# Kernel tuning notes

Measured on AMD Instinct MI355X. Metric: run time of the kernel, lower is better.

The kernel has to match this reference:

```python
import jax, jax.numpy as jnp
import numpy as np

N_EMBD = 768
N_HEAD = 12
HEAD_DIM = N_EMBD // N_HEAD
B, T = 2, 2048
EPS = 1e-5


def setup_inputs() -> dict:
    key = jax.random.key(0)
    ks = jax.random.split(key, 16)
    s = 0.02
    return {
        "x": jax.random.normal(ks[0], (B, T, N_EMBD), dtype=jnp.float32),
        "ln1_g": jnp.ones((N_EMBD,), jnp.float32),
        "ln1_b": jnp.zeros((N_EMBD,), jnp.float32),
        "W_attn": jax.random.normal(ks[1], (N_EMBD, 3 * N_EMBD), jnp.float32) * s,
        "b_attn": jnp.zeros((3 * N_EMBD,), jnp.float32),
        "W_cproj": jax.random.normal(ks[2], (N_EMBD, N_EMBD), jnp.float32) * s,
        "b_cproj": jnp.zeros((N_EMBD,), jnp.float32),
        "ln2_g": jnp.ones((N_EMBD,), jnp.float32),
        "ln2_b": jnp.zeros((N_EMBD,), jnp.float32),
        "W_fc": jax.random.normal(ks[3], (N_EMBD, 4 * N_EMBD), jnp.float32) * s,
        "b_fc": jnp.zeros((4 * N_EMBD,), jnp.float32),
        "W_mproj": jax.random.normal(ks[4], (4 * N_EMBD, N_EMBD), jnp.float32) * s,
        "b_mproj": jnp.zeros((N_EMBD,), jnp.float32),
    }


def _layernorm(x, g, b):
    mu = jnp.mean(x, axis=-1, keepdims=True)
    var = jnp.mean(jnp.square(x - mu), axis=-1, keepdims=True)
    return (x - mu) * jax.lax.rsqrt(var + EPS) * g + b


def _attention(h, W_attn, b_attn, W_cproj, b_cproj):
    Bx, Tx, C = h.shape
    qkv = h @ W_attn + b_attn  # [B, T, 3C]
    q, k, v = jnp.split(qkv, 3, axis=-1)
    # [B, H, T, D]
    def split_heads(t):
        return t.reshape(Bx, Tx, N_HEAD, HEAD_DIM).transpose(0, 2, 1, 3)
    q, k, v = split_heads(q), split_heads(k), split_heads(v)
    att = jnp.einsum("bhqd,bhkd->bhqk", q, k) / np.sqrt(HEAD_DIM).astype(np.float32)
    causal = jnp.tril(jnp.ones((Tx, Tx), dtype=bool))
    att = jnp.where(causal, att, jnp.float32(-jnp.inf))
    att = jax.nn.softmax(att, axis=-1)
    y = jnp.einsum("bhqk,bhkd->bhqd", att, v)
    y = y.transpose(0, 2, 1, 3).reshape(Bx, Tx, C)
    return y @ W_cproj + b_cproj


def _mlp(h, W_fc, b_fc, W_mproj, b_mproj):
    return jax.nn.gelu(h @ W_fc + b_fc, approximate=False) @ W_mproj + b_mproj


def reference(x, ln1_g, ln1_b, W_attn, b_attn, W_cproj, b_cproj,
              ln2_g, ln2_b, W_fc, b_fc, W_mproj, b_mproj):
    x = x + _attention(_layernorm(x, ln1_g, ln1_b), W_attn, b_attn, W_cproj, b_cproj)
    x = x + _mlp(_layernorm(x, ln2_g, ln2_b), W_fc, b_fc, W_mproj, b_mproj)
    return x
```

## Files before the change

### kernel.cpp

```cpp
#include <hip/hip_runtime.h>
#include <cstdint>
#include <cstddef>

#define B_ 2
#define T_ 2048
#define C_ 768
#define H_ 12
#define D_ 64

typedef __attribute__((ext_vector_type(8))) short s16x8;
typedef __attribute__((ext_vector_type(4))) float fx4;

static __device__ __forceinline__ unsigned short f2bf(float f) {
  unsigned u = __builtin_bit_cast(unsigned, f);
  unsigned r = u + 0x7fffu + ((u >> 16) & 1u);
  return (unsigned short)(r >> 16);
}
static __device__ __forceinline__ unsigned short f2bf_trunc(float f) {
  return (unsigned short)(__builtin_bit_cast(unsigned, f) >> 16);
}

static __device__ __forceinline__ void glds16(const unsigned short* g, unsigned short* l) {
  __builtin_amdgcn_global_load_lds(
      (const __attribute__((address_space(1))) void*)(g),
      (__attribute__((address_space(3))) void*)(l), 16, 0, 0);
}

__global__ __launch_bounds__(256) void transpose_cast(
    const float* __restrict__ W, unsigned short* __restrict__ Wt, int R, int C) {
  __shared__ float tile[32][33];
  int tx = threadIdx.x & 31;
  int ty = threadIdx.x >> 5;
  int c0 = blockIdx.x * 32, r0 = blockIdx.y * 32;
#pragma unroll
  for (int i = 0; i < 4; ++i)
    tile[ty + i * 8][tx] = W[(size_t)(r0 + ty + i * 8) * C + (c0 + tx)];
  __syncthreads();
#pragma unroll
  for (int i = 0; i < 4; ++i)
    Wt[(size_t)(c0 + ty + i * 8) * R + (r0 + tx)] = f2bf(tile[tx][ty + i * 8]);
}

__global__ __launch_bounds__(256) void layernorm_bf16(
    const float* __restrict__ X, const float* __restrict__ g,
    const float* __restrict__ bb, unsigned short* __restrict__ O) {
  int row = blockIdx.x, tid = threadIdx.x;
  const float* xr = X + (size_t)row * C_;
  float v0 = xr[tid], v1 = xr[tid + 256], v2 = xr[tid + 512];
  float s = v0 + v1 + v2;
  float s2 = v0 * v0 + v1 * v1 + v2 * v2;
#pragma unroll
  for (int off = 1; off < 64; off <<= 1) {
    s += __shfl_xor(s, off);
    s2 += __shfl_xor(s2, off);
  }
  __shared__ float ps[8];
  int wv = tid >> 6;
  if ((tid & 63) == 0) { ps[wv] = s; ps[wv + 4] = s2; }
  __syncthreads();
  s = ps[0] + ps[1] + ps[2] + ps[3];
  s2 = ps[4] + ps[5] + ps[6] + ps[7];
  float mu = s * (1.f / C_);
  float var = s2 * (1.f / C_) - mu * mu;
  float rstd = rsqrtf(var + 1e-5f);
  unsigned short* orow = O + (size_t)row * C_;
  orow[tid]       = f2bf((v0 - mu) * rstd * g[tid]       + bb[tid]);
  orow[tid + 256] = f2bf((v1 - mu) * rstd * g[tid + 256] + bb[tid + 256]);
  orow[tid + 512] = f2bf((v2 - mu) * rstd * g[tid + 512] + bb[tid + 512]);
}

template <int BM, int BN, int BK, int MODE>
__global__ __launch_bounds__(256) void gemm_db(
    const unsigned short* __restrict__ A, const unsigned short* __restrict__ Bt,
    const float* __restrict__ bias, const float* __restrict__ resid,
    float* __restrict__ outF, unsigned short* __restrict__ outB,
    unsigned short* __restrict__ qO, unsigned short* __restrict__ kO,
    unsigned short* __restrict__ vtO, int M, int N, int K) {
  constexpr int AT = BM / 32;
  constexpr int BT = BN / 32;
  constexpr int KS = BK / 32;
  constexpr int CA = BM * BK / 2048;
  constexpr int CB = BN * BK / 2048;
  constexpr int ASZ = BM * BK, BSZ = BN * BK;
  constexpr bool SWIZ = (BK == 64);
  __shared__ __align__(16) unsigned short As[2 * ASZ];
  __shared__ __align__(16) unsigned short Bs[2 * BSZ];
  int tid = threadIdx.x;
  int wv = tid >> 6, lane = tid & 63, quad = lane >> 4, l15 = lane & 15;
  int wm = wv >> 1, wn = wv & 1;
  int m0, n0;
  if (MODE == 1) { m0 = blockIdx.x * BM; n0 = blockIdx.y * BN; }
  else           { n0 = blockIdx.x * BN; m0 = blockIdx.y * BM; }
  fx4 acc[AT][BT];
#pragma unroll
  for (int i = 0; i < AT; ++i)
#pragma unroll
    for (int j = 0; j < BT; ++j) acc[i][j] = fx4{0.f, 0.f, 0.f, 0.f};

  int nk = K / BK;
#pragma unroll
  for (int i = 0; i < CA; ++i) {
    int e = (i * 256 + tid) * 8;
    int row = e / BK, col = e & (BK - 1);
    if (SWIZ) col = (((col >> 3) ^ (row & 7)) << 3);
    glds16(&A[(size_t)(m0 + row) * K + col], &As[(i * 256 + (tid & ~63)) * 8]);
  }
#pragma unroll
  for (int i = 0; i < CB; ++i) {
    int e = (i * 256 + tid) * 8;
    int row = e / BK, col = e & (BK - 1);
    if (SWIZ) col = (((col >> 3) ^ (row & 7)) << 3);
    glds16(&Bt[(size_t)(n0 + row) * K + col], &Bs[(i * 256 + (tid & ~63)) * 8]);
  }
  for (int kt = 0; kt < nk; ++kt) {
    int cur = kt & 1;
    __syncthreads();
    if (kt + 1 < nk) {
      int kb = (kt + 1) * BK;
      int nxt = cur ^ 1;
#pragma unroll
      for (int i = 0; i < CA; ++i) {
        int e = (i * 256 + tid) * 8;
        int row = e / BK, col = e & (BK - 1);
        if (SWIZ) col = (((col >> 3) ^ (row & 7)) << 3);
        glds16(&A[(size_t)(m0 + row) * K + kb + col],
               &As[nxt * ASZ + (i * 256 + (tid & ~63)) * 8]);
      }
#pragma unroll
      for (int i = 0; i < CB; ++i) {
        int e = (i * 256 + tid) * 8;
        int row = e / BK, col = e & (BK - 1);
        if (SWIZ) col = (((col >> 3) ^ (row & 7)) << 3);
        glds16(&Bt[(size_t)(n0 + row) * K + kb + col],
               &Bs[nxt * BSZ + (i * 256 + (tid & ~63)) * 8]);
      }
    }
#pragma unroll
    for (int ks = 0; ks < KS; ++ks) {
      s16x8 af[AT], bf[BT];
#pragma unroll
      for (int mt = 0; mt < AT; ++mt) {
        int r = wm * (BM / 2) + mt * 16 + l15;
        int c = ks * 32 + quad * 8;
        if (SWIZ) c = (((c >> 3) ^ (r & 7)) << 3);
        af[mt] = *(const s16x8*)&As[cur * ASZ + r * BK + c];
      }
#pragma unroll
      for (int nt = 0; nt < BT; ++nt) {
        int r = wn * (BN / 2) + nt * 16 + l15;
        int c = ks * 32 + quad * 8;
        if (SWIZ) c = (((c >> 3) ^ (r & 7)) << 3);
        bf[nt] = *(const s16x8*)&Bs[cur * BSZ + r * BK + c];
      }
#pragma unroll
      for (int mt = 0; mt < AT; ++mt)
#pragma unroll
        for (int nt = 0; nt < BT; ++nt)
          acc[mt][nt] = __builtin_amdgcn_mfma_f32_16x16x32_bf16(af[mt], bf[nt], acc[mt][nt], 0, 0, 0);
    }
  }

#pragma unroll
  for (int mt = 0; mt < AT; ++mt)
#pragma unroll
    for (int nt = 0; nt < BT; ++nt) {
      int mb = m0 + wm * (BM / 2) + mt * 16 + quad * 4;
      int n = n0 + wn * (BN / 2) + nt * 16 + l15;
      if (MODE == 0) {
        int which = n / C_;
        int within = n - which * C_;
        int hd = within >> 6, d = within & 63;
        int bbx = mb >> 11, t = mb & 2047;
        size_t bh = (size_t)(bbx * H_ + hd);
        float b = bias[n];
        if (which == 2) {
          unsigned v01 = (unsigned)f2bf(acc[mt][nt][0] + b) |
                         ((unsigned)f2bf(acc[mt][nt][1] + b) << 16);
          unsigned v23 = (unsigned)f2bf(acc[mt][nt][2] + b) |
                         ((unsigned)f2bf(acc[mt][nt][3] + b) << 16);
          *(uint2*)&vtO[(bh * D_ + d) * T_ + t] = uint2{v01, v23};
        } else {
          unsigned short* dst = (which == 0) ? qO : kO;
#pragma unroll
          for (int r = 0; r < 4; ++r)
            dst[(bh * T_ + t + r) * D_ + d] = f2bf(acc[mt][nt][r] + b);
        }
      } else if (MODE == 1) {
#pragma unroll
        for (int r = 0; r < 4; ++r) {
          int m = mb + r;
          float v = acc[mt][nt][r] + bias[n];
          outF[(size_t)m * N + n] = resid[(size_t)m * N + n] + v;
        }
      } else {
#pragma unroll
        for (int r = 0; r < 4; ++r) {
          int m = mb + r;
          float v = acc[mt][nt][r] + bias[n];
          float gl = 0.5f * v * (1.f + erff(v * 0.70710678118654752f));
          outB[(size_t)m * N + n] = f2bf(gl);
        }
      }
    }
}

__global__ __launch_bounds__(256) void attn_fused(
    const unsigned short* __restrict__ Q, const unsigned short* __restrict__ Kg,
    const unsigned short* __restrict__ Vt, unsigned short* __restrict__ Y) {
  __shared__ __align__(16) unsigned short Ks[64 * 72];
  __shared__ __align__(16) unsigned short Vs[64 * 72];
  __shared__ __align__(16) unsigned short Ps[4][16 * 72];
  int tid = threadIdx.x;
  int wv = tid >> 6, lane = tid & 63, quad = lane >> 4, l15 = lane & 15;
  int l = blockIdx.x;
  int w = l >> 8, c = l & 255;
  int i = c & 31;
  int bh = w * 8 + (c >> 5);
  int qt;
  if (w == 0)      qt = i;
  else if (w == 1) qt = (i + 16) & 31;
  else             qt = (i < 16) ? (30 - 2 * i) : (63 - 2 * i);
  int bbx = bh / H_, hh = bh - bbx * H_;
  int q0 = qt * 64;
  size_t base = (size_t)bh * T_ * D_;
  size_t vbase = (size_t)bh * D_ * T_;
  int qrow = q0 + wv * 16 + l15;
  s16x8 qf0 = *(const s16x8*)&Q[base + (size_t)qrow * D_ + quad * 8];
  s16x8 qf1 = *(const s16x8*)&Q[base + (size_t)qrow * D_ + 32 + quad * 8];
  float lsum[4];
  fx4 oacc[4];
#pragma unroll
  for (int t = 0; t < 4; ++t) {
    lsum[t] = 0.f;
    oacc[t] = fx4{0.f, 0.f, 0.f, 0.f};
  }
  int r0s = tid >> 3;
  int c8 = (tid & 7) * 8;
  uint4 ka, kc, va, vc;
  {
    ka = *(const uint4*)&Kg[base + (size_t)r0s * D_ + c8];
    kc = *(const uint4*)&Kg[base + (size_t)(r0s + 32) * D_ + c8];
    va = *(const uint4*)&Vt[vbase + (size_t)r0s * T_ + c8];
    vc = *(const uint4*)&Vt[vbase + (size_t)(r0s + 32) * T_ + c8];
  }
  for (int kb = 0; kb <= qt; ++kb) {
    int k0 = kb * 64;
    __syncthreads();
    *(uint4*)&Ks[r0s * 72 + c8] = ka;
    *(uint4*)&Ks[(r0s + 32) * 72 + c8] = kc;
    *(uint4*)&Vs[r0s * 72 + c8] = va;
    *(uint4*)&Vs[(r0s + 32) * 72 + c8] = vc;
    __syncthreads();
    if (kb < qt) {
      int kn = k0 + 64;
      ka = *(const uint4*)&Kg[base + (size_t)(kn + r0s) * D_ + c8];
      kc = *(const uint4*)&Kg[base + (size_t)(kn + r0s + 32) * D_ + c8];
      va = *(const uint4*)&Vt[vbase + (size_t)r0s * T_ + kn + c8];
      vc = *(const uint4*)&Vt[vbase + (size_t)(r0s + 32) * T_ + kn + c8];
    }
    fx4 sc[4];
#pragma unroll
    for (int nt = 0; nt < 4; ++nt) {
      sc[nt] = fx4{0.f, 0.f, 0.f, 0.f};
      s16x8 kf0 = *(const s16x8*)&Ks[(nt * 16 + l15) * 72 + quad * 8];
      s16x8 kf1 = *(const s16x8*)&Ks[(nt * 16 + l15) * 72 + 32 + quad * 8];
      sc[nt] = __builtin_amdgcn_mfma_f32_16x16x32_bf16(qf0, kf0, sc[nt], 0, 0, 0);
      sc[nt] = __builtin_amdgcn_mfma_f32_16x16x32_bf16(qf1, kf1, sc[nt], 0, 0, 0);
    }
    bool diag = (kb == qt);
    unsigned short* pw = &Ps[wv][0];
#pragma unroll
    for (int nt = 0; nt < 4; ++nt)
#pragma unroll
      for (int r = 0; r < 4; ++r) {
        float p;
        if (diag && (k0 + nt * 16 + l15) > (q0 + wv * 16 + quad * 4 + r)) {
          p = 0.f;
        } else {
          p = __expf(sc[nt][r] * 0.125f);
        }
        lsum[r] += p;
        pw[(quad * 4 + r) * 72 + nt * 16 + l15] = f2bf_trunc(p);
      }
    s16x8 pa0 = *(const s16x8*)&pw[l15 * 72 + quad * 8];
    s16x8 pa1 = *(const s16x8*)&pw[l15 * 72 + 32 + quad * 8];
#pragma unroll
    for (int nt = 0; nt < 4; ++nt) {
      s16x8 vf0 = *(const s16x8*)&Vs[(nt * 16 + l15) * 72 + quad * 8];
      s16x8 vf1 = *(const s16x8*)&Vs[(nt * 16 + l15) * 72 + 32 + quad * 8];
      oacc[nt] = __builtin_amdgcn_mfma_f32_16x16x32_bf16(pa0, vf0, oacc[nt], 0, 0, 0);
      oacc[nt] = __builtin_amdgcn_mfma_f32_16x16x32_bf16(pa1, vf1, oacc[nt], 0, 0, 0);
    }
  }
#pragma unroll
  for (int r = 0; r < 4; ++r) {
#pragma unroll
    for (int off = 1; off < 16; off <<= 1) lsum[r] += __shfl_xor(lsum[r], off);
  }
#pragma unroll
  for (int nt = 0; nt < 4; ++nt)
#pragma unroll
    for (int r = 0; r < 4; ++r) {
      float o = oacc[nt][r] / lsum[r];
      int token = bbx * T_ + q0 + wv * 16 + quad * 4 + r;
      Y[(size_t)token * C_ + hh * D_ + nt * 16 + l15] = f2bf(o);
    }
}

extern "C" void kernel_launch(void* const* d_in, const int* in_sizes, int n_in,
                              void* d_out, int out_size, void* d_ws, size_t ws_size,
                              hipStream_t stream) {
  const float* x      = (const float*)d_in[0];
  const float* ln1g   = (const float*)d_in[1];
  const float* ln1b   = (const float*)d_in[2];
  const float* Wattn  = (const float*)d_in[3];
  const float* battn  = (const float*)d_in[4];
  const float* Wcproj = (const float*)d_in[5];
  const float* bcproj = (const float*)d_in[6];
  const float* ln2g   = (const float*)d_in[7];
  const float* ln2b   = (const float*)d_in[8];
  const float* Wfc    = (const float*)d_in[9];
  const float* bfc    = (const float*)d_in[10];
  const float* Wmproj = (const float*)d_in[11];
  const float* bmproj = (const float*)d_in[12];
  float* out = (float*)d_out;
  char* ws = (char*)d_ws;

  unsigned short* WattnT  = (unsigned short*)(ws + 0);
  unsigned short* WcprojT = (unsigned short*)(ws + 3538944);
  unsigned short* WfcT    = (unsigned short*)(ws + 4718592);
  unsigned short* WmprojT = (unsigned short*)(ws + 9437184);
  unsigned short* hbuf    = (unsigned short*)(ws + 14155776);
  unsigned short* Qb      = (unsigned short*)(ws + 20447232);
  unsigned short* Kb      = (unsigned short*)(ws + 26738688);
  unsigned short* Vtb     = (unsigned short*)(ws + 33030144);
  unsigned short* Yb      = (unsigned short*)(ws + 39321600);
  float*          x1      = (float*)(ws + 45613056);
  unsigned short* Ab      = (unsigned short*)(ws + 58195968);

  transpose_cast<<<dim3(2304 / 32, 768 / 32), 256, 0, stream>>>(Wattn, WattnT, 768, 2304);
  transpose_cast<<<dim3(768 / 32, 768 / 32), 256, 0, stream>>>(Wcproj, WcprojT, 768, 768);
  transpose_cast<<<dim3(3072 / 32, 768 / 32), 256, 0, stream>>>(Wfc, WfcT, 768, 3072);
  transpose_cast<<<dim3(768 / 32, 3072 / 32), 256, 0, stream>>>(Wmproj, WmprojT, 3072, 768);

  layernorm_bf16<<<4096, 256, 0, stream>>>(x, ln1g, ln1b, hbuf);

  gemm_db<128, 128, 32, 0><<<dim3(2304 / 128, 4096 / 128), 256, 0, stream>>>(
      hbuf, WattnT, battn, nullptr, nullptr, nullptr, Qb, Kb, Vtb, 4096, 2304, 768);

  attn_fused<<<768, 256, 0, stream>>>(Qb, Kb, Vtb, Yb);

  gemm_db<128, 64, 64, 1><<<dim3(4096 / 128, 768 / 64), 256, 0, stream>>>(
      Yb, WcprojT, bcproj, x, x1, nullptr, nullptr, nullptr, nullptr, 4096, 768, 768);

  layernorm_bf16<<<4096, 256, 0, stream>>>(x1, ln2g, ln2b, hbuf);

  gemm_db<128, 128, 32, 2><<<dim3(3072 / 128, 4096 / 128), 256, 0, stream>>>(
      hbuf, WfcT, bfc, nullptr, nullptr, Ab, nullptr, nullptr, nullptr, 4096, 3072, 768);

  gemm_db<128, 64, 64, 1><<<dim3(4096 / 128, 768 / 64), 256, 0, stream>>>(
      Ab, WmprojT, bmproj, x1, out, nullptr, nullptr, nullptr, nullptr, 4096, 768, 3072);
}
```

Before: 272.1 us.

## Merge weight transposes and first layernorm into one prep kernel; retune GEMM tiles

Folds the four weight transpose-cast launches and the first layernorm into a single kernel that picks its job from the block index. This cuts launch count and lets the small jobs overlap on the GPU. Separately, the QKV, c_proj and m_proj GEMMs switch to 128x96x64 tiles with matching grids, changing the tile count and wave balance across CUs. The risk is that the new tile shapes interact badly with the gemm template's thread mapping or register use.

Measured after the change: 271.2 us. No clear change (-0.3%).

```diff
diff --git a/kernel.cpp b/kernel.cpp
--- a/kernel.cpp
+++ b/kernel.cpp
@@ -26,19 +26,56 @@
       (__attribute__((address_space(3))) void*)(l), 16, 0, 0);
 }
 
-__global__ __launch_bounds__(256) void transpose_cast(
-    const float* __restrict__ W, unsigned short* __restrict__ Wt, int R, int C) {
+__global__ __launch_bounds__(256) void prep(
+    const float* __restrict__ Wattn, const float* __restrict__ Wcproj,
+    const float* __restrict__ Wfc, const float* __restrict__ Wmproj,
+    unsigned short* __restrict__ WattnT, unsigned short* __restrict__ WcprojT,
+    unsigned short* __restrict__ WfcT, unsigned short* __restrict__ WmprojT,
+    const float* __restrict__ X, const float* __restrict__ g,
+    const float* __restrict__ bb, unsigned short* __restrict__ O) {
   __shared__ float tile[32][33];
-  int tx = threadIdx.x & 31;
-  int ty = threadIdx.x >> 5;
-  int c0 = blockIdx.x * 32, r0 = blockIdx.y * 32;
-#pragma unroll
-  for (int i = 0; i < 4; ++i)
-    tile[ty + i * 8][tx] = W[(size_t)(r0 + ty + i * 8) * C + (c0 + tx)];
-  __syncthreads();
-#pragma unroll
-  for (int i = 0; i < 4; ++i)
-    Wt[(size_t)(c0 + ty + i * 8) * R + (r0 + tx)] = f2bf(tile[tx][ty + i * 8]);
+  __shared__ float ps[8];
+  int bid = blockIdx.x, tid = threadIdx.x;
+  if (bid < 6912) {
+    const float* W; unsigned short* Wt; int R, C, idx;
+    if (bid < 1728)      { W = Wattn;  Wt = WattnT;  R = 768;  C = 2304; idx = bid; }
+    else if (bid < 2304) { W = Wcproj; Wt = WcprojT; R = 768;  C = 768;  idx = bid - 1728; }
+    else if (bid < 4608) { W = Wfc;    Wt = WfcT;    R = 768;  C = 3072; idx = bid - 2304; }
+    else                 { W = Wmproj; Wt = WmprojT; R = 3072; C = 768;  idx = bid - 4608; }
+    int ct = C >> 5;
+    int c0 = (idx % ct) * 32, r0 = (idx / ct) * 32;
+    int tx = tid & 31, ty = tid >> 5;
+#pragma unroll
+    for (int i = 0; i < 4; ++i)
+      tile[ty + i * 8][tx] = W[(size_t)(r0 + ty + i * 8) * C + (c0 + tx)];
+    __syncthreads();
+#pragma unroll
+    for (int i = 0; i < 4; ++i)
+      Wt[(size_t)(c0 + ty + i * 8) * R + (r0 + tx)] = f2bf(tile[tx][ty + i * 8]);
+  } else {
+    int row = bid - 6912;
+    const float* xr = X + (size_t)row * C_;
+    float v0 = xr[tid], v1 = xr[tid + 256], v2 = xr[tid + 512];
+    float s = v0 + v1 + v2;
+    float s2 = v0 * v0 + v1 * v1 + v2 * v2;
+#pragma unroll
+    for (int off = 1; off < 64; off <<= 1) {
+      s += __shfl_xor(s, off);
+      s2 += __shfl_xor(s2, off);
+    }
+    int wv = tid >> 6;
+    if ((tid & 63) == 0) { ps[wv] = s; ps[wv + 4] = s2; }
+    __syncthreads();
+    s = ps[0] + ps[1] + ps[2] + ps[3];
+    s2 = ps[4] + ps[5] + ps[6] + ps[7];
+    float mu = s * (1.f / C_);
+    float var = s2 * (1.f / C_) - mu * mu;
+    float rstd = rsqrtf(var + 1e-5f);
+    unsigned short* orow = O + (size_t)row * C_;
+    orow[tid]       = f2bf((v0 - mu) * rstd * g[tid]       + bb[tid]);
+    orow[tid + 256] = f2bf((v1 - mu) * rstd * g[tid + 256] + bb[tid + 256]);
+    orow[tid + 512] = f2bf((v2 - mu) * rstd * g[tid + 512] + bb[tid + 512]);
+  }
 }
 
 __global__ __launch_bounds__(256) void layernorm_bf16(
@@ -338,26 +375,23 @@
   float*          x1      = (float*)(ws + 45613056);
   unsigned short* Ab      = (unsigned short*)(ws + 58195968);
 
-  transpose_cast<<<dim3(2304 / 32, 768 / 32), 256, 0, stream>>>(Wattn, WattnT, 768, 2304);
-  transpose_cast<<<dim3(768 / 32, 768 / 32), 256, 0, stream>>>(Wcproj, WcprojT, 768, 768);
-  transpose_cast<<<dim3(3072 / 32, 768 / 32), 256, 0, stream>>>(Wfc, WfcT, 768, 3072);
-  transpose_cast<<<dim3(768 / 32, 3072 / 32), 256, 0, stream>>>(Wmproj, WmprojT, 3072, 768);
-
-  layernorm_bf16<<<4096, 256, 0, stream>>>(x, ln1g, ln1b, hbuf);
-
-  gemm_db<128, 128, 32, 0><<<dim3(2304 / 128, 4096 / 128), 256, 0, stream>>>(
+  prep<<<11008, 256, 0, stream>>>(Wattn, Wcproj, Wfc, Wmproj,
+                                  WattnT, WcprojT, WfcT, WmprojT,
+                                  x, ln1g, ln1b, hbuf);
+
+  gemm_db<128, 96, 64, 0><<<dim3(24, 32), 256, 0, stream>>>(
       hbuf, WattnT, battn, nullptr, nullptr, nullptr, Qb, Kb, Vtb, 4096, 2304, 768);
 
   attn_fused<<<768, 256, 0, stream>>>(Qb, Kb, Vtb, Yb);
 
-  gemm_db<128, 64, 64, 1><<<dim3(4096 / 128, 768 / 64), 256, 0, stream>>>(
+  gemm_db<128, 96, 64, 1><<<dim3(32, 8), 256, 0, stream>>>(
       Yb, WcprojT, bcproj, x, x1, nullptr, nullptr, nullptr, nullptr, 4096, 768, 768);
 
   layernorm_bf16<<<4096, 256, 0, stream>>>(x1, ln2g, ln2b, hbuf);
 
-  gemm_db<128, 128, 32, 2><<<dim3(3072 / 128, 4096 / 128), 256, 0, stream>>>(
+  gemm_db<128, 128, 32, 2><<<dim3(24, 32), 256, 0, stream>>>(
       hbuf, WfcT, bfc, nullptr, nullptr, Ab, nullptr, nullptr, nullptr, 4096, 3072, 768);
 
-  gemm_db<128, 64, 64, 1><<<dim3(4096 / 128, 768 / 64), 256, 0, stream>>>(
+  gemm_db<128, 96, 64, 1><<<dim3(32, 8), 256, 0, stream>>>(
       Ab, WmprojT, bmproj, x1, out, nullptr, nullptr, nullptr, nullptr, 4096, 768, 3072);
 }
```
